# Optimization experiments

Measured on AMD Instinct MI355X. Metric: run time of the kernel, lower is better.

## Reference

```python
import jax, jax.numpy as jnp
import numpy as np

MAX_SEGMENTS = 256
MAX_PIXELS = 400   # fixed-capacity bucket per segment
EMBED_DIM = 768
N_CHANNELS = 3


def setup_inputs() -> dict:
    key = jax.random.key(0)
    k1, k2, k3, k4 = jax.random.split(key, 4)
    img = jax.random.normal(k1, (32, N_CHANNELS, 384, 384), dtype=jnp.float32)
    segments = jax.random.randint(k2, (32, 384, 384), 0, MAX_SEGMENTS, dtype=jnp.int32)
    fan_in = N_CHANNELS * MAX_PIXELS
    proj_w = jax.random.normal(k3, (EMBED_DIM, fan_in), dtype=jnp.float32) / np.sqrt(fan_in).astype(np.float32)
    proj_b = jax.random.normal(k4, (EMBED_DIM,), dtype=jnp.float32) * 0.01
    return {"img": img, "segments": segments, "proj_w": proj_w, "proj_b": proj_b}


def _bucketize(img_flat, seg_flat):
    """img_flat: [C, N] pixels in row-major scan order; seg_flat: [N] int ids.
    Returns [S, C*P]: first P pixels (scan order) of each segment, zero padded,
    channel-major per segment — matching torch's masked gather + flatten."""
    C, N = img_flat.shape
    idx = jnp.arange(N, dtype=jnp.int32)
    # stable sort by segment id preserves scan order within each segment
    order = jnp.argsort(seg_flat, stable=True)
    sorted_seg = seg_flat[order]
    is_start = jnp.concatenate([jnp.ones((1,), bool), sorted_seg[1:] != sorted_seg[:-1]])
    group_start = jax.lax.cummax(jnp.where(is_start, idx, 0))
    rank_sorted = idx - group_start                      # position within segment
    rank = jnp.zeros((N,), jnp.int32).at[order].set(rank_sorted)
    dump = MAX_SEGMENTS * MAX_PIXELS                      # overflow slot (discarded)
    dest = jnp.where(rank < MAX_PIXELS, seg_flat.astype(jnp.int32) * MAX_PIXELS + rank, dump)
    buf = jnp.zeros((C, dump + 1), img_flat.dtype).at[:, dest].set(img_flat)
    # [C, S, P] -> [S, C, P] -> [S, C*P] (channel-major flatten per segment)
    return buf[:, :dump].reshape(C, MAX_SEGMENTS, MAX_PIXELS).transpose(1, 0, 2).reshape(MAX_SEGMENTS, C * MAX_PIXELS)


def reference(img, segments, proj_w, proj_b):
    B, C, H, W = img.shape
    feats = jax.vmap(_bucketize)(img.reshape(B, C, H * W), segments.reshape(B, H * W))
    # [B, S, C*P] @ [C*P, E] + [E]
    return feats @ proj_w.T + proj_b
```

## Files before the change

kernel.cpp:

```cpp
#include <hip/hip_runtime.h>
#include <hip/hip_bf16.h>
#include <cstdint>

#define BATCH 32
#define NCH 3
#define HW 147456
#define NSEG 256
#define NPIX 400
#define KDIM 1200
#define EDIM 768
#define MROWS (BATCH * NSEG)

#define CHUNK 4096
#define NCHUNK (HW / CHUNK)
#define SUB 1024

#define ROW_BYTES 4800
#define APK_BYTES ((size_t)MROWS * ROW_BYTES)
#define W_BYTES (EDIM * KDIM * 4)

typedef __attribute__((ext_vector_type(8))) short short8b;
typedef __attribute__((ext_vector_type(16))) float f32x16;

__device__ __forceinline__ uint32_t bf16_rn(float f) {
    uint32_t u = __float_as_uint(f);
    return (u + 0x7fffu + ((u >> 16) & 1u)) >> 16;
}
__device__ __forceinline__ float bf16_tof(uint32_t h) { return __uint_as_float(h << 16); }
__device__ __forceinline__ uint32_t pack_split(float v) {
    uint32_t hi = bf16_rn(v);
    uint32_t lo = bf16_rn(v - bf16_tof(hi));
    return (lo << 16) | hi;
}

__device__ __forceinline__ void async_copy16(const void* gsrc, void* ldst) {
    __builtin_amdgcn_global_load_lds(
        (const __attribute__((address_space(1))) uint32_t*)gsrc,
        (__attribute__((address_space(3))) uint32_t*)ldst, 16, 0, 0);
}

__global__ __launch_bounds__(256) void hist_kernel(const int* __restrict__ seg,
                                                   int* __restrict__ cnt) {
    __shared__ int h[NSEG];
    const int tid = threadIdx.x;
    h[tid] = 0;
    __syncthreads();
    const int blk = blockIdx.x;
    const int b = blk / NCHUNK, ck = blk % NCHUNK;
    const int* segb = seg + (size_t)b * HW + ck * CHUNK;
#pragma unroll
    for (int i = 0; i < CHUNK / 256; ++i) atomicAdd(&h[segb[i * 256 + tid]], 1);
    __syncthreads();
    cnt[blk * NSEG + tid] = h[tid];
}

__global__ __launch_bounds__(256) void scan_kernel(int* __restrict__ cnt) {
    const int t = blockIdx.x * 256 + threadIdx.x;
    const int b = t >> 8, s = t & 255;
    int run = 0;
#pragma unroll
    for (int ck = 0; ck < NCHUNK; ++ck) {
        int* p = cnt + ((size_t)(b * NCHUNK + ck)) * NSEG + s;
        int v = *p;
        *p = run;
        run += v;
    }
    cnt[(size_t)(b * NCHUNK) * NSEG + s] = run;
}

__global__ __launch_bounds__(256) void scatter_kernel(const float* __restrict__ img,
                                                      const int* __restrict__ seg,
                                                      const int* __restrict__ base,
                                                      uint32_t* __restrict__ apk) {
    __shared__ int wpos[4][NSEG];
    __shared__ int sl[NSEG];
    __shared__ uint32_t st0[CHUNK], st1[CHUNK], st2[CHUNK];

    const int tid = threadIdx.x;
    const int lane = tid & 63;
    const int wid = tid >> 6;
    const int blk = blockIdx.x;
    const int b = blk / NCHUNK, ck = blk % NCHUNK;

    const int sb = (ck == 0) ? 0 : base[(size_t)blk * NSEG + tid];
    wpos[0][tid] = 0; wpos[1][tid] = 0; wpos[2][tid] = 0; wpos[3][tid] = 0;
    __syncthreads();

    const int* segb = seg + (size_t)b * HW;
    const float* imgb = img + (size_t)b * NCH * HW;
    const int startp = ck * CHUNK + wid * SUB;
    const unsigned long long lt = (lane == 0) ? 0ull : ((~0ull) >> (64 - lane));

    int sv[16];
    unsigned long long mv[16];
#pragma unroll
    for (int g = 0; g < 16; ++g) {
        const int p = startp + g * 64 + lane;
        const int s = segb[p];
        unsigned long long m = ~0ull;
#pragma unroll
        for (int bit = 0; bit < 8; ++bit) {
            unsigned long long bal = __ballot((s >> bit) & 1);
            m &= ((s >> bit) & 1) ? bal : ~bal;
        }
        sv[g] = s; mv[g] = m;
        if ((m & lt) == 0ull) atomicAdd(&wpos[wid][s], __popcll(m));
    }
    __syncthreads();

    int csum;
    {
        const int s = tid;
        int r = sb;
        int t0 = wpos[0][s]; wpos[0][s] = r; r += t0;
        int t1 = wpos[1][s]; wpos[1][s] = r; r += t1;
        int t2 = wpos[2][s]; wpos[2][s] = r; r += t2;
        int t3 = wpos[3][s]; wpos[3][s] = r; r += t3;
        csum = r - sb;
        sl[s] = csum;
    }
    __syncthreads();
#pragma unroll
    for (int off = 1; off < NSEG; off <<= 1) {
        int y = (tid >= off) ? sl[tid - off] : 0;
        __syncthreads();
        sl[tid] += y;
        __syncthreads();
    }
    {
        const int excl = sl[tid] - csum;
        __syncthreads();
        sl[tid] = (sb << 13) | excl;
    }
    __syncthreads();

#pragma unroll
    for (int g = 0; g < 16; ++g) {
        const int p = startp + g * 64 + lane;
        const int s = sv[g];
        const unsigned long long m = mv[g];
        const int rig = __popcll(m & lt);
        const int leader = __ffsll((unsigned long long)m) - 1;
        int old = 0;
        if (rig == 0) old = atomicAdd(&wpos[wid][s], __popcll(m));
        old = __shfl(old, leader, 64);
        const int rank = old + rig;
        const int v = sl[s];
        const int j = rank - (v >> 13) + (v & 8191);
        st0[j] = pack_split(imgb[p]);
        st1[j] = pack_split(imgb[HW + p]);
        st2[j] = pack_split(imgb[2 * HW + p]);
    }
    __syncthreads();

    uint32_t* apkb = apk + (size_t)b * NSEG * (ROW_BYTES / 4);
#pragma unroll
    for (int it = 0; it < CHUNK / 256; ++it) {
        const int j = it * 256 + tid;
        int s = 0;
#pragma unroll
        for (int step = 128; step; step >>= 1) {
            const int c = s + step;
            if (c < NSEG && (sl[c] & 8191) <= j) s = c;
        }
        const int v = sl[s];
        const int rank = (v >> 13) + (j - (v & 8191));
        if (rank < NPIX) {
            uint32_t* dst = apkb + (size_t)s * (ROW_BYTES / 4) + rank;
            dst[0]            = st0[j];
            dst[NPIX]         = st1[j];
            dst[2 * NPIX]     = st2[j];
        }
    }
}

__global__ __launch_bounds__(256) void repackA_kernel(uint32_t* __restrict__ apk,
                                                      const int* __restrict__ cnt) {
    __shared__ uint32_t buf[4][KDIM];
    const int tid = threadIdx.x;
    const int l = tid & 63;
    const int wid = tid >> 6;
    const int row = blockIdx.x * 4 + wid;
    const int b = row >> 8, s = row & 255;
    int tot = cnt[(size_t)(b * NCHUNK) * NSEG + s];
    if (tot > NPIX) tot = NPIX;

    uint32_t* rowp = apk + (size_t)row * (ROW_BYTES / 4);
#pragma unroll
    for (int i = 0; i < 19; ++i) {
        const int idx = i * 64 + l;
        if (idx < KDIM) buf[wid][idx] = rowp[idx];
    }
    __syncthreads();
#pragma unroll
    for (int i = 0; i < 10; ++i) {
        const int j = i * 64 + l;
        if (j < KDIM / 2) {
            const int k0 = 2 * j, k1 = 2 * j + 1;
            const int r0 = k0 - ((k0 * 41) >> 14) * 400;
            const int r1 = k1 - ((k1 * 41) >> 14) * 400;
            const uint32_t p0 = (r0 < tot) ? buf[wid][k0] : 0u;
            const uint32_t p1 = (r1 < tot) ? buf[wid][k1] : 0u;
            rowp[j]             = (p0 & 0xffffu) | (p1 << 16);
            rowp[KDIM / 2 + j]  = (p0 >> 16) | (p1 & 0xffff0000u);
        }
    }
}

__global__ __launch_bounds__(256) void repackW_kernel(float* __restrict__ w) {
    __shared__ float buf[4][KDIM];
    const int tid = threadIdx.x;
    const int l = tid & 63;
    const int wid = tid >> 6;
    const int row = blockIdx.x * 4 + wid;
    float* rowp = w + (size_t)row * KDIM;
#pragma unroll
    for (int i = 0; i < 19; ++i) {
        const int idx = i * 64 + l;
        if (idx < KDIM) buf[wid][idx] = rowp[idx];
    }
    __syncthreads();
    uint32_t* rowu = (uint32_t*)rowp;
#pragma unroll
    for (int i = 0; i < 10; ++i) {
        const int j = i * 64 + l;
        if (j < KDIM / 2) {
            const float f0 = buf[wid][2 * j], f1 = buf[wid][2 * j + 1];
            const uint32_t h0 = bf16_rn(f0), h1 = bf16_rn(f1);
            const uint32_t l0 = bf16_rn(f0 - bf16_tof(h0));
            const uint32_t l1 = bf16_rn(f1 - bf16_tof(h1));
            rowu[j]            = h0 | (h1 << 16);
            rowu[KDIM / 2 + j] = l0 | (l1 << 16);
        }
    }
}

__global__ __launch_bounds__(128) void gemm_kernel(const uint8_t* __restrict__ A,
                                                   const uint8_t* __restrict__ Wp,
                                                   const float* __restrict__ bias,
                                                   float* __restrict__ out) {
    __shared__ uint8_t smem[49152];

    const int tid = threadIdx.x;
    const int l = tid & 63;
    const int wid = tid >> 6;

    const int bid = blockIdx.x;
    const int xcd = bid & 7;
    const int t = bid >> 3;
    const int bn = t % 12;
    const int bm = (t / 12) * 8 + xcd;

    const int swzl = ((l & 7) * 16) ^ ((l >> 3) << 4);
    const int xread = (l & 7) << 4;

    const uint8_t* Abase = A + (size_t)bm * 128 * ROW_BYTES;

    f32x16 acc[2][2] = {};

    for (int k0 = 0; k0 < KDIM; k0 += 64) {
#pragma unroll
        for (int ii = 0; ii < 8; ++ii) {
            const int i = wid * 8 + ii;
            const int row = i * 8 + (l >> 3);
            const size_t gb = (size_t)row * ROW_BYTES + k0 * 2 + swzl;
            async_copy16(Abase + gb,        smem + i * 1024);
            async_copy16(Abase + gb + 2400, smem + 16384 + i * 1024);
        }
#pragma unroll
        for (int ii = 0; ii < 4; ++ii) {
            const int i = wid * 4 + ii;
            const int row = i * 8 + (l >> 3);
            const size_t gb = (size_t)(bn * 64 + row) * ROW_BYTES + k0 * 2 + swzl;
            async_copy16(Wp + gb, smem + 32768 + i * 1024);
            size_t gl = gb + 2400;
            if (gl + 16 > (size_t)W_BYTES) gl = 0;
            async_copy16(Wp + gl, smem + 40960 + i * 1024);
        }
        __syncthreads();

#pragma unroll
        for (int ks = 0; ks < 4; ++ks) {
            if (k0 + ks * 16 >= KDIM) break;
            const int koff = ks * 32 + ((l >> 5) * 16);
            short8b ahi[2], alo[2], bhi[2], blo[2];
#pragma unroll
            for (int mi = 0; mi < 2; ++mi) {
                const int row = wid * 64 + mi * 32 + (l & 31);
                const int byteA = row * 128 + (koff ^ xread);
                ahi[mi] = *(const short8b*)(smem + byteA);
                alo[mi] = *(const short8b*)(smem + 16384 + byteA);
            }
#pragma unroll
            for (int ni = 0; ni < 2; ++ni) {
                const int row = ni * 32 + (l & 31);
                const int byteB = row * 128 + (koff ^ xread);
                bhi[ni] = *(const short8b*)(smem + 32768 + byteB);
                blo[ni] = *(const short8b*)(smem + 40960 + byteB);
            }
#pragma unroll
            for (int mi = 0; mi < 2; ++mi)
#pragma unroll
                for (int ni = 0; ni < 2; ++ni) {
                    acc[mi][ni] = __builtin_amdgcn_mfma_f32_32x32x16_bf16(ahi[mi], bhi[ni], acc[mi][ni], 0, 0, 0);
                    acc[mi][ni] = __builtin_amdgcn_mfma_f32_32x32x16_bf16(ahi[mi], blo[ni], acc[mi][ni], 0, 0, 0);
                    acc[mi][ni] = __builtin_amdgcn_mfma_f32_32x32x16_bf16(alo[mi], bhi[ni], acc[mi][ni], 0, 0, 0);
                }
        }
        __syncthreads();
    }

#pragma unroll
    for (int ni = 0; ni < 2; ++ni) {
        const int e = bn * 64 + ni * 32 + (l & 31);
        const float bv = bias[e];
#pragma unroll
        for (int mi = 0; mi < 2; ++mi) {
            const int rbase = bm * 128 + wid * 64 + mi * 32 + 4 * (l >> 5);
#pragma unroll
            for (int r = 0; r < 16; ++r) {
                const int row = rbase + (r & 3) + 8 * (r >> 2);
                out[(size_t)row * EDIM + e] = acc[mi][ni][r] + bv;
            }
        }
    }
}

extern "C" void kernel_launch(void* const* d_in, const int* in_sizes, int n_in,
                              void* d_out, int out_size, void* d_ws, size_t ws_size,
                              hipStream_t stream) {
    const float* img      = (const float*)d_in[0];
    const int*   segments = (const int*)d_in[1];
    float*       proj_w   = (float*)d_in[2];
    const float* proj_b   = (const float*)d_in[3];
    float* out = (float*)d_out;

    uint32_t* apk = (uint32_t*)d_ws;
    int*      cnt = (int*)((char*)d_ws + APK_BYTES);

    hist_kernel<<<BATCH * NCHUNK, 256, 0, stream>>>(segments, cnt);
    scan_kernel<<<MROWS / 256, 256, 0, stream>>>(cnt);
    repackW_kernel<<<EDIM / 4, 256, 0, stream>>>(proj_w);
    scatter_kernel<<<BATCH * NCHUNK, 256, 0, stream>>>(img, segments, cnt, apk);
    repackA_kernel<<<MROWS / 4, 256, 0, stream>>>(apk, cnt);

    gemm_kernel<<<64 * 12, 128, 0, stream>>>((const uint8_t*)apk, (const uint8_t*)proj_w,
                                             proj_b, out);
}
```

Baseline: 260.9 us.

## Write split bf16 layout directly in scatter, replace repack with tail zeroing

The scatter kernel now emits the hi/lo bf16 planes in the final GEMM layout, so the full-row repackA pass becomes a small kernel that only zeroes the unfilled tail of each segment row. The scatter kernel grows to 8 waves per block, and the GEMM moves to 4 waves in a 2x2 arrangement per tile. This removes a full read/write pass over the A buffer. In exchange, scatter stores become 16-bit and more fragmented.

Measured after the change: 224.8 us. 1.16x faster.

```diff
diff --git a/kernel.cpp b/kernel.cpp
--- a/kernel.cpp
+++ b/kernel.cpp
@@ -13,7 +13,8 @@
 
 #define CHUNK 4096
 #define NCHUNK (HW / CHUNK)
-#define SUB 1024
+#define NW 8
+#define SUBW (CHUNK / NW)
 
 #define ROW_BYTES 4800
 #define APK_BYTES ((size_t)MROWS * ROW_BYTES)
@@ -68,11 +69,11 @@
     cnt[(size_t)(b * NCHUNK) * NSEG + s] = run;
 }
 
-__global__ __launch_bounds__(256) void scatter_kernel(const float* __restrict__ img,
+__global__ __launch_bounds__(512) void scatter_kernel(const float* __restrict__ img,
                                                       const int* __restrict__ seg,
                                                       const int* __restrict__ base,
-                                                      uint32_t* __restrict__ apk) {
-    __shared__ int wpos[4][NSEG];
+                                                      uint8_t* __restrict__ apk) {
+    __shared__ int wpos[NW][NSEG];
     __shared__ int sl[NSEG];
     __shared__ uint32_t st0[CHUNK], st1[CHUNK], st2[CHUNK];
 
@@ -82,19 +83,21 @@
     const int blk = blockIdx.x;
     const int b = blk / NCHUNK, ck = blk % NCHUNK;
 
-    const int sb = (ck == 0) ? 0 : base[(size_t)blk * NSEG + tid];
-    wpos[0][tid] = 0; wpos[1][tid] = 0; wpos[2][tid] = 0; wpos[3][tid] = 0;
+    int sb = 0;
+    if (tid < NSEG) sb = (ck == 0) ? 0 : base[(size_t)blk * NSEG + tid];
+#pragma unroll
+    for (int i = 0; i < (NW * NSEG) / 512; ++i) ((int*)wpos)[i * 512 + tid] = 0;
     __syncthreads();
 
     const int* segb = seg + (size_t)b * HW;
     const float* imgb = img + (size_t)b * NCH * HW;
-    const int startp = ck * CHUNK + wid * SUB;
+    const int startp = ck * CHUNK + wid * SUBW;
     const unsigned long long lt = (lane == 0) ? 0ull : ((~0ull) >> (64 - lane));
 
-    int sv[16];
-    unsigned long long mv[16];
-#pragma unroll
-    for (int g = 0; g < 16; ++g) {
+    int sv[SUBW / 64];
+    unsigned long long mv[SUBW / 64];
+#pragma unroll
+    for (int g = 0; g < SUBW / 64; ++g) {
         const int p = startp + g * 64 + lane;
         const int s = segb[p];
         unsigned long long m = ~0ull;
@@ -108,34 +111,37 @@
     }
     __syncthreads();
 
-    int csum;
+    int csum = 0;
+    if (tid < NSEG) {
+        int r = sb;
+#pragma unroll
+        for (int w = 0; w < NW; ++w) {
+            const int t = wpos[w][tid];
+            wpos[w][tid] = r;
+            r += t;
+        }
+        csum = r - sb;
+        sl[tid] = csum;
+    }
+    __syncthreads();
+#pragma unroll
+    for (int off = 1; off < NSEG; off <<= 1) {
+        int y = 0;
+        if (tid < NSEG && tid >= off) y = sl[tid - off];
+        __syncthreads();
+        if (tid < NSEG) sl[tid] += y;
+        __syncthreads();
+    }
     {
-        const int s = tid;
-        int r = sb;
-        int t0 = wpos[0][s]; wpos[0][s] = r; r += t0;
-        int t1 = wpos[1][s]; wpos[1][s] = r; r += t1;
-        int t2 = wpos[2][s]; wpos[2][s] = r; r += t2;
-        int t3 = wpos[3][s]; wpos[3][s] = r; r += t3;
-        csum = r - sb;
-        sl[s] = csum;
-    }
-    __syncthreads();
-#pragma unroll
-    for (int off = 1; off < NSEG; off <<= 1) {
-        int y = (tid >= off) ? sl[tid - off] : 0;
-        __syncthreads();
-        sl[tid] += y;
-        __syncthreads();
-    }
-    {
-        const int excl = sl[tid] - csum;
-        __syncthreads();
-        sl[tid] = (sb << 13) | excl;
-    }
-    __syncthreads();
-
-#pragma unroll
-    for (int g = 0; g < 16; ++g) {
+        int excl = 0;
+        if (tid < NSEG) excl = sl[tid] - csum;
+        __syncthreads();
+        if (tid < NSEG) sl[tid] = (sb << 13) | excl;
+    }
+    __syncthreads();
+
+#pragma unroll
+    for (int g = 0; g < SUBW / 64; ++g) {
         const int p = startp + g * 64 + lane;
         const int s = sv[g];
         const unsigned long long m = mv[g];
@@ -153,10 +159,10 @@
     }
     __syncthreads();
 
-    uint32_t* apkb = apk + (size_t)b * NSEG * (ROW_BYTES / 4);
-#pragma unroll
-    for (int it = 0; it < CHUNK / 256; ++it) {
-        const int j = it * 256 + tid;
+    uint8_t* apkb = apk + (size_t)b * NSEG * ROW_BYTES;
+#pragma unroll
+    for (int it = 0; it < CHUNK / 512; ++it) {
+        const int j = it * 512 + tid;
         int s = 0;
 #pragma unroll
         for (int step = 128; step; step >>= 1) {
@@ -166,44 +172,31 @@
         const int v = sl[s];
         const int rank = (v >> 13) + (j - (v & 8191));
         if (rank < NPIX) {
-            uint32_t* dst = apkb + (size_t)s * (ROW_BYTES / 4) + rank;
-            dst[0]            = st0[j];
-            dst[NPIX]         = st1[j];
-            dst[2 * NPIX]     = st2[j];
-        }
-    }
-}
-
-__global__ __launch_bounds__(256) void repackA_kernel(uint32_t* __restrict__ apk,
-                                                      const int* __restrict__ cnt) {
-    __shared__ uint32_t buf[4][KDIM];
+            uint16_t* hp = (uint16_t*)(apkb + (size_t)s * ROW_BYTES);
+            uint16_t* lp = (uint16_t*)(apkb + (size_t)s * ROW_BYTES + 2400);
+            const uint32_t v0 = st0[j], v1 = st1[j], v2 = st2[j];
+            hp[rank]       = (uint16_t)v0;  lp[rank]       = (uint16_t)(v0 >> 16);
+            hp[400 + rank] = (uint16_t)v1;  lp[400 + rank] = (uint16_t)(v1 >> 16);
+            hp[800 + rank] = (uint16_t)v2;  lp[800 + rank] = (uint16_t)(v2 >> 16);
+        }
+    }
+}
+
+__global__ __launch_bounds__(256) void tailzero_kernel(uint8_t* __restrict__ apk,
+                                                       const int* __restrict__ cnt) {
     const int tid = threadIdx.x;
     const int l = tid & 63;
     const int wid = tid >> 6;
     const int row = blockIdx.x * 4 + wid;
     const int b = row >> 8, s = row & 255;
-    int tot = cnt[(size_t)(b * NCHUNK) * NSEG + s];
-    if (tot > NPIX) tot = NPIX;
-
-    uint32_t* rowp = apk + (size_t)row * (ROW_BYTES / 4);
-#pragma unroll
-    for (int i = 0; i < 19; ++i) {
-        const int idx = i * 64 + l;
-        if (idx < KDIM) buf[wid][idx] = rowp[idx];
-    }
-    __syncthreads();
-#pragma unroll
-    for (int i = 0; i < 10; ++i) {
-        const int j = i * 64 + l;
-        if (j < KDIM / 2) {
-            const int k0 = 2 * j, k1 = 2 * j + 1;
-            const int r0 = k0 - ((k0 * 41) >> 14) * 400;
-            const int r1 = k1 - ((k1 * 41) >> 14) * 400;
-            const uint32_t p0 = (r0 < tot) ? buf[wid][k0] : 0u;
-            const uint32_t p1 = (r1 < tot) ? buf[wid][k1] : 0u;
-            rowp[j]             = (p0 & 0xffffu) | (p1 << 16);
-            rowp[KDIM / 2 + j]  = (p0 >> 16) | (p1 & 0xffff0000u);
-        }
+    const int tot = cnt[(size_t)(b * NCHUNK) * NSEG + s];
+    if (tot >= NPIX) return;
+    uint16_t* hp = (uint16_t*)(apk + (size_t)row * ROW_BYTES);
+    uint16_t* lp = (uint16_t*)(apk + (size_t)row * ROW_BYTES + 2400);
+    for (int r = tot + l; r < NPIX; r += 64) {
+        hp[r] = 0; lp[r] = 0;
+        hp[400 + r] = 0; lp[400 + r] = 0;
+        hp[800 + r] = 0; lp[800 + r] = 0;
     }
 }
 
@@ -235,7 +228,7 @@
     }
 }
 
-__global__ __launch_bounds__(128) void gemm_kernel(const uint8_t* __restrict__ A,
+__global__ __launch_bounds__(256) void gemm_kernel(const uint8_t* __restrict__ A,
                                                    const uint8_t* __restrict__ Wp,
                                                    const float* __restrict__ bias,
                                                    float* __restrict__ out) {
@@ -244,6 +237,7 @@
     const int tid = threadIdx.x;
     const int l = tid & 63;
     const int wid = tid >> 6;
+    const int wm = wid >> 1, wn = wid & 1;
 
     const int bid = blockIdx.x;
     const int xcd = bid & 7;
@@ -256,20 +250,20 @@
 
     const uint8_t* Abase = A + (size_t)bm * 128 * ROW_BYTES;
 
-    f32x16 acc[2][2] = {};
+    f32x16 acc[2] = {};
 
     for (int k0 = 0; k0 < KDIM; k0 += 64) {
 #pragma unroll
-        for (int ii = 0; ii < 8; ++ii) {
-            const int i = wid * 8 + ii;
+        for (int ii = 0; ii < 4; ++ii) {
+            const int i = wid * 4 + ii;
             const int row = i * 8 + (l >> 3);
             const size_t gb = (size_t)row * ROW_BYTES + k0 * 2 + swzl;
             async_copy16(Abase + gb,        smem + i * 1024);
             async_copy16(Abase + gb + 2400, smem + 16384 + i * 1024);
         }
 #pragma unroll
-        for (int ii = 0; ii < 4; ++ii) {
-            const int i = wid * 4 + ii;
+        for (int ii = 0; ii < 2; ++ii) {
+            const int i = wid * 2 + ii;
             const int row = i * 8 + (l >> 3);
             const size_t gb = (size_t)(bn * 64 + row) * ROW_BYTES + k0 * 2 + swzl;
             async_copy16(Wp + gb, smem + 32768 + i * 1024);
@@ -283,45 +277,39 @@
         for (int ks = 0; ks < 4; ++ks) {
             if (k0 + ks * 16 >= KDIM) break;
             const int koff = ks * 32 + ((l >> 5) * 16);
-            short8b ahi[2], alo[2], bhi[2], blo[2];
+            short8b ahi[2], alo[2], bhi, blo;
 #pragma unroll
             for (int mi = 0; mi < 2; ++mi) {
-                const int row = wid * 64 + mi * 32 + (l & 31);
+                const int row = wm * 64 + mi * 32 + (l & 31);
                 const int byteA = row * 128 + (koff ^ xread);
                 ahi[mi] = *(const short8b*)(smem + byteA);
                 alo[mi] = *(const short8b*)(smem + 16384 + byteA);
             }
-#pragma unroll
-            for (int ni = 0; ni < 2; ++ni) {
-                const int row = ni * 32 + (l & 31);
+            {
+                const int row = wn * 32 + (l & 31);
                 const int byteB = row * 128 + (koff ^ xread);
-                bhi[ni] = *(const short8b*)(smem + 32768 + byteB);
-                blo[ni] = *(const short8b*)(smem + 40960 + byteB);
+                bhi = *(const short8b*)(smem + 32768 + byteB);
+                blo = *(const short8b*)(smem + 40960 + byteB);
             }
 #pragma unroll
-            for (int mi = 0; mi < 2; ++mi)
-#pragma unroll
-                for (int ni = 0; ni < 2; ++ni) {
-                    acc[mi][ni] = __builtin_amdgcn_mfma_f32_32x32x16_bf16(ahi[mi], bhi[ni], acc[mi][ni], 0, 0, 0);
-                    acc[mi][ni] = __builtin_amdgcn_mfma_f32_32x32x16_bf16(ahi[mi], blo[ni], acc[mi][ni], 0, 0, 0);
-                    acc[mi][ni] = __builtin_amdgcn_mfma_f32_32x32x16_bf16(alo[mi], bhi[ni], acc[mi][ni], 0, 0, 0);
-                }
-        }
-        __syncthreads();
-    }
-
-#pragma unroll
-    for (int ni = 0; ni < 2; ++ni) {
-        const int e = bn * 64 + ni * 32 + (l & 31);
-        const float bv = bias[e];
-#pragma unroll
-        for (int mi = 0; mi < 2; ++mi) {
-            const int rbase = bm * 128 + wid * 64 + mi * 32 + 4 * (l >> 5);
-#pragma unroll
-            for (int r = 0; r < 16; ++r) {
-                const int row = rbase + (r & 3) + 8 * (r >> 2);
-                out[(size_t)row * EDIM + e] = acc[mi][ni][r] + bv;
+            for (int mi = 0; mi < 2; ++mi) {
+                acc[mi] = __builtin_amdgcn_mfma_f32_32x32x16_bf16(ahi[mi], bhi, acc[mi], 0, 0, 0);
+                acc[mi] = __builtin_amdgcn_mfma_f32_32x32x16_bf16(ahi[mi], blo, acc[mi], 0, 0, 0);
+                acc[mi] = __builtin_amdgcn_mfma_f32_32x32x16_bf16(alo[mi], bhi, acc[mi], 0, 0, 0);
             }
+        }
+        __syncthreads();
+    }
+
+    const int e = bn * 64 + wn * 32 + (l & 31);
+    const float bv = bias[e];
+#pragma unroll
+    for (int mi = 0; mi < 2; ++mi) {
+        const int rbase = bm * 128 + wm * 64 + mi * 32 + 4 * (l >> 5);
+#pragma unroll
+        for (int r = 0; r < 16; ++r) {
+            const int row = rbase + (r & 3) + 8 * (r >> 2);
+            out[(size_t)row * EDIM + e] = acc[mi][r] + bv;
         }
     }
 }
@@ -335,15 +323,14 @@
     const float* proj_b   = (const float*)d_in[3];
     float* out = (float*)d_out;
 
-    uint32_t* apk = (uint32_t*)d_ws;
-    int*      cnt = (int*)((char*)d_ws + APK_BYTES);
+    uint8_t* apk = (uint8_t*)d_ws;
+    int*     cnt = (int*)((char*)d_ws + APK_BYTES);
 
     hist_kernel<<<BATCH * NCHUNK, 256, 0, stream>>>(segments, cnt);
     scan_kernel<<<MROWS / 256, 256, 0, stream>>>(cnt);
     repackW_kernel<<<EDIM / 4, 256, 0, stream>>>(proj_w);
-    scatter_kernel<<<BATCH * NCHUNK, 256, 0, stream>>>(img, segments, cnt, apk);
-    repackA_kernel<<<MROWS / 4, 256, 0, stream>>>(apk, cnt);
-
-    gemm_kernel<<<64 * 12, 128, 0, stream>>>((const uint8_t*)apk, (const uint8_t*)proj_w,
-                                             proj_b, out);
-}
+    scatter_kernel<<<BATCH * NCHUNK, 512, 0, stream>>>(img, segments, cnt, apk);
+    tailzero_kernel<<<MROWS / 4, 256, 0, stream>>>(apk, cnt);
+
+    gemm_kernel<<<64 * 12, 256, 0, stream>>>(apk, (const uint8_t*)proj_w, proj_b, out);
+}
```
